# Kernel tuning notes

Hardware: AMD Instinct MI355X
Metric: run time of the kernel (lower is better)

Reference implementation:

```python
import jax, jax.numpy as jnp
import numpy as np

TOP_K = 8
ROUTED_SCALING_FACTOR = 2.5
NORM_TOPK_PROB = True


def setup_inputs() -> dict:
    key = jax.random.key(0)
    k1, k2 = jax.random.split(key)
    hidden_states = jax.random.normal(k1, (4, 4096, 4096), dtype=jnp.float32)
    # gate weight: (n_routed_experts, hidden_size)
    weight = jax.random.normal(k2, (256, 4096), dtype=jnp.float32) * (1.0 / np.sqrt(4096))
    return {"hidden_states": hidden_states, "weight": weight}


def reference(hidden_states, weight):
    bsz, seq_len, h = hidden_states.shape
    x = hidden_states.reshape(-1, h).astype(jnp.float32)  # [T, h]
    # gate logits: [T, E]
    logits = jnp.einsum("th,eh->te", x, weight.astype(jnp.float32))
    scores = jax.nn.softmax(logits, axis=-1)
    topk_weight, topk_idx = jax.lax.top_k(scores, TOP_K)  # [T, k]
    if TOP_K > 1 and NORM_TOPK_PROB:
        denom = jnp.sum(topk_weight, axis=-1, keepdims=True) + 1e-20
        topk_weight = topk_weight / denom * ROUTED_SCALING_FACTOR
    else:
        topk_weight = topk_weight * ROUTED_SCALING_FACTOR
    return (topk_idx, topk_weight)
```

## Files before the change

kernel.cpp:

```cpp
#include <hip/hip_runtime.h>
#include <math.h>

typedef _Float16 half8  __attribute__((ext_vector_type(8)));
typedef _Float16 half4v __attribute__((ext_vector_type(4)));
typedef float    f32x16 __attribute__((ext_vector_type(16)));

namespace {
constexpr int H      = 4096;
constexpr int E      = 256;
constexpr int TOPK   = 8;
constexpr int NCAND  = 12;
constexpr int BM     = 64;
constexpr int BK     = 32;
constexpr int NCHUNK = H / BK;
constexpr int SLD    = E + 4;
constexpr float DELTA = 5e-4f;
constexpr size_t WF_BYTES = (size_t)E * H * 2 * 2;
constexpr int SMEM_BYTES = BM * SLD * 4;
}

__global__ void convert_w_kernel(const float* __restrict__ W,
                                 _Float16* __restrict__ Wf) {
    int t  = blockIdx.x * blockDim.x + threadIdx.x;
    int e  = t >> 10;
    int kq = t & 1023;
    float4 w4 = *(const float4*)(W + ((size_t)e << 12) + (kq << 2));
    float x0 = w4.x * 64.0f, x1 = w4.y * 64.0f, x2 = w4.z * 64.0f, x3 = w4.w * 64.0f;
    _Float16 h0 = (_Float16)x0, h1 = (_Float16)x1, h2 = (_Float16)x2, h3 = (_Float16)x3;
    _Float16 l0 = (_Float16)(x0 - (float)h0), l1 = (_Float16)(x1 - (float)h1);
    _Float16 l2 = (_Float16)(x2 - (float)h2), l3 = (_Float16)(x3 - (float)h3);
    int k    = kq << 2;
    int nt   = e >> 5;
    int ks   = k >> 4;
    int lane = (e & 31) | (((k >> 3) & 1) << 5);
    int j    = k & 7;
    size_t base = (((size_t)nt * 256 + ks) * 2) * 512 + lane * 8 + j;
    half4v hv = {h0, h1, h2, h3};
    half4v lv = {l0, l1, l2, l3};
    *(half4v*)(Wf + base)       = hv;
    *(half4v*)(Wf + base + 512) = lv;
}

struct BF { half8 h[2][2]; half8 l[2][2]; };

__global__ __launch_bounds__(512, 2)
void moe_gate_mfma(const float* __restrict__ X, const _Float16* __restrict__ Wf,
                   const float* __restrict__ Wg,
                   float* __restrict__ out_idx, float* __restrict__ out_w) {
    __shared__ __align__(16) char smem[SMEM_BYTES];
    _Float16* Abuf = (_Float16*)smem;
    float*    sc   = (float*)smem;

    const int tid  = threadIdx.x;
    const int lane = tid & 63;
    const int wave = tid >> 6;
    const int wr   = wave >> 2;
    const int wc   = wave & 3;
    const int m0   = blockIdx.x * BM;

    const int m_s  = tid >> 3;
    const int kq_s = tid & 7;
    const int ks_s = kq_s >> 2;
    const int mt_s = m_s >> 5;
    const int ln_s = (m_s & 31) | (((kq_s >> 1) & 1) << 5);
    const int j_s  = (kq_s & 1) * 4;
    const int dst_s = ((ks_s * 2 + mt_s) * 2) * 512 + ln_s * 8 + j_s;
    const float* xgp = X + (size_t)(m0 + m_s) * H + kq_s * 4;

    f32x16 acc[2];
    #pragma unroll
    for (int nt = 0; nt < 2; ++nt)
        #pragma unroll
        for (int r = 0; r < 16; ++r) acc[nt][r] = 0.0f;

    auto load_b = [&](int kc, BF& b) {
        #pragma unroll
        for (int ks = 0; ks < 2; ++ks)
            #pragma unroll
            for (int nt = 0; nt < 2; ++nt) {
                size_t base = (((size_t)(2 * wc + nt) * 256 + (kc * 2 + ks)) * 2) * 512
                              + lane * 8;
                b.h[ks][nt] = *(const half8*)(Wf + base);
                b.l[ks][nt] = *(const half8*)(Wf + base + 512);
            }
    };
    auto stage = [&](int bufIdx, float4 xv) {
        _Float16* buf = Abuf + bufIdx * 4096;
        float x0 = xv.x, x1 = xv.y, x2 = xv.z, x3 = xv.w;
        _Float16 h0 = (_Float16)x0, h1 = (_Float16)x1, h2 = (_Float16)x2, h3 = (_Float16)x3;
        _Float16 l0 = (_Float16)(x0 - (float)h0), l1 = (_Float16)(x1 - (float)h1);
        _Float16 l2 = (_Float16)(x2 - (float)h2), l3 = (_Float16)(x3 - (float)h3);
        half4v hv = {h0, h1, h2, h3};
        half4v lv = {l0, l1, l2, l3};
        *(half4v*)(buf + dst_s)       = hv;
        *(half4v*)(buf + dst_s + 512) = lv;
    };
    auto compute = [&](int bufIdx, const BF& b) {
        const _Float16* buf = Abuf + bufIdx * 4096;
        #pragma unroll
        for (int ks = 0; ks < 2; ++ks) {
            const _Float16* p = buf + (ks * 2 + wr) * 1024 + lane * 8;
            half8 a_hi = *(const half8*)p;
            half8 a_lo = *(const half8*)(p + 512);
            #pragma unroll
            for (int nt = 0; nt < 2; ++nt) {
                acc[nt] = __builtin_amdgcn_mfma_f32_32x32x16_f16(a_hi, b.h[ks][nt], acc[nt], 0, 0, 0);
                acc[nt] = __builtin_amdgcn_mfma_f32_32x32x16_f16(a_lo, b.h[ks][nt], acc[nt], 0, 0, 0);
                acc[nt] = __builtin_amdgcn_mfma_f32_32x32x16_f16(a_hi, b.l[ks][nt], acc[nt], 0, 0, 0);
            }
        }
    };

    BF bcur;
    load_b(0, bcur);
    float4 xv = *(const float4*)(xgp);
    stage(0, xv);
    __syncthreads();
    float4 xnxt = *(const float4*)(xgp + BK);

    for (int kc = 0; kc < NCHUNK; ++kc) {
        BF bnxt;
        float4 xfar = make_float4(0.f, 0.f, 0.f, 0.f);
        if (kc + 1 < NCHUNK) load_b(kc + 1, bnxt);
        if (kc + 2 < NCHUNK) xfar = *(const float4*)(xgp + (size_t)(kc + 2) * BK);
        compute(kc & 1, bcur);
        if (kc + 1 < NCHUNK) {
            stage((kc + 1) & 1, xnxt);
            asm volatile("s_waitcnt lgkmcnt(0)" ::: "memory");
            __builtin_amdgcn_s_barrier();
        }
        bcur = bnxt;
        xnxt = xfar;
    }

    __syncthreads();
    #pragma unroll
    for (int nt = 0; nt < 2; ++nt) {
        #pragma unroll
        for (int r = 0; r < 16; ++r) {
            int row = (r & 3) + 8 * (r >> 2) + 4 * (lane >> 5);
            int col = lane & 31;
            sc[(wr * 32 + row) * SLD + wc * 64 + nt * 32 + col] = acc[nt][r] * 0.015625f;
        }
    }
    __syncthreads();

    for (int t8 = 0; t8 < 8; ++t8) {
        const int t = wave * 8 + t8;
        float4 pv = *(const float4*)(sc + t * SLD + lane * 4);
        float p0 = pv.x, p1 = pv.y, p2 = pv.z, p3 = pv.w;

        float tv[NCAND]; int ti[NCAND];
        #pragma unroll
        for (int s = 0; s < NCAND; ++s) {
            float bv = p0; int bi = lane * 4;
            if (p1 > bv || (p1 == bv && lane * 4 + 1 < bi)) { bv = p1; bi = lane * 4 + 1; }
            if (p2 > bv || (p2 == bv && lane * 4 + 2 < bi)) { bv = p2; bi = lane * 4 + 2; }
            if (p3 > bv || (p3 == bv && lane * 4 + 3 < bi)) { bv = p3; bi = lane * 4 + 3; }
            #pragma unroll
            for (int off = 32; off > 0; off >>= 1) {
                float ov = __shfl_xor(bv, off, 64);
                int   oi = __shfl_xor(bi, off, 64);
                if (ov > bv || (ov == bv && oi < bi)) { bv = ov; bi = oi; }
            }
            tv[s] = bv; ti[s] = bi;
            if ((bi >> 2) == lane) {
                const int sl = bi & 3;
                if      (sl == 0) p0 = -3e38f;
                else if (sl == 1) p1 = -3e38f;
                else if (sl == 2) p2 = -3e38f;
                else              p3 = -3e38f;
            }
        }

        bool rescue = false;
        #pragma unroll
        for (int g = 0; g < 9; ++g) rescue |= (tv[g] - tv[g + 1] < DELTA);

        if (rescue) {
            double dv[NCAND];
            const float* xr = X + (size_t)(m0 + t) * H;
            #pragma unroll 1
            for (int c = 0; c < NCAND; ++c) {
                const float* wrow = Wg + (size_t)ti[c] * H;
                double s_ = 0.0;
                #pragma unroll
                for (int it = 0; it < 16; ++it) {
                    float4 xa = *(const float4*)(xr + it * 256 + lane * 4);
                    float4 wa = *(const float4*)(wrow + it * 256 + lane * 4);
                    s_ += (double)xa.x * wa.x + (double)xa.y * wa.y
                        + (double)xa.z * wa.z + (double)xa.w * wa.w;
                }
                #pragma unroll
                for (int off = 32; off > 0; off >>= 1) s_ += __shfl_xor(s_, off, 64);
                dv[c] = s_;
            }
            int si[NCAND];
            #pragma unroll
            for (int c = 0; c < NCAND; ++c) si[c] = ti[c];
            #pragma unroll
            for (int a = 0; a < TOPK; ++a) {
                int best = a;
                #pragma unroll
                for (int b = a + 1; b < NCAND; ++b) {
                    if (dv[b] > dv[best] || (dv[b] == dv[best] && si[b] < si[best])) best = b;
                }
                double tdv = dv[a]; dv[a] = dv[best]; dv[best] = tdv;
                int    tsi = si[a]; si[a] = si[best]; si[best] = tsi;
            }
            #pragma unroll
            for (int s = 0; s < TOPK; ++s) { tv[s] = (float)dv[s]; ti[s] = si[s]; }
        }

        if (lane == 0) {
            float M = tv[0];
            float e8[TOPK]; float den = 0.0f;
            #pragma unroll
            for (int s = 0; s < TOPK; ++s) { e8[s] = expf(tv[s] - M); den += e8[s]; }
            float scl = 2.5f / den;
            size_t tok = (size_t)(m0 + t);
            #pragma unroll
            for (int s = 0; s < TOPK; ++s) {
                out_idx[tok * TOPK + s] = (float)ti[s];
                out_w[tok * TOPK + s]   = e8[s] * scl;
            }
        }
    }
}

namespace fb {
constexpr int BM = 32, BK = 32;
constexpr int XS_LD = BM + 4, WS_LD = E + 4;
constexpr int LDS_FLOATS = BK * XS_LD + BK * WS_LD;
}

__global__ __launch_bounds__(256, 2)
void moe_gate_fallback(const float* __restrict__ X, const float* __restrict__ W,
                       float* __restrict__ out_idx, float* __restrict__ out_w) {
    __shared__ float lds[fb::LDS_FLOATS];
    float* xs = lds;
    float* ws = lds + fb::BK * fb::XS_LD;
    const int tid = threadIdx.x;
    const int tx = tid & 31, ty = tid >> 5;
    const int m0 = blockIdx.x * fb::BM;
    float acc[4][8];
    #pragma unroll
    for (int i = 0; i < 4; ++i)
        #pragma unroll
        for (int j = 0; j < 8; ++j) acc[i][j] = 0.0f;
    const int lr = tid >> 3, lc = (tid & 7) * 4;
    const float* xg = X + (size_t)(m0 + lr) * H + lc;
    const float* wg = W + (size_t)lr * H + lc;
    for (int kc = 0; kc < H; kc += fb::BK) {
        float4 xv = *(const float4*)(xg + kc);
        float4 wv[8];
        #pragma unroll
        for (int i = 0; i < 8; ++i) wv[i] = *(const float4*)(wg + (size_t)i * 32 * H + kc);
        __syncthreads();
        #pragma unroll
        for (int j = 0; j < 4; ++j) xs[(lc + j) * fb::XS_LD + lr] = ((const float*)&xv)[j];
        #pragma unroll
        for (int i = 0; i < 8; ++i)
            #pragma unroll
            for (int j = 0; j < 4; ++j)
                ws[(lc + j) * fb::WS_LD + i * 32 + lr] = ((const float*)&wv[i])[j];
        __syncthreads();
        #pragma unroll
        for (int kk = 0; kk < fb::BK; ++kk) {
            float4 xa = *(const float4*)(xs + kk * fb::XS_LD + ty * 4);
            float4 wb0 = *(const float4*)(ws + kk * fb::WS_LD + tx * 8);
            float4 wb1 = *(const float4*)(ws + kk * fb::WS_LD + tx * 8 + 4);
            const float xr[4] = {xa.x, xa.y, xa.z, xa.w};
            const float wr8[8] = {wb0.x, wb0.y, wb0.z, wb0.w, wb1.x, wb1.y, wb1.z, wb1.w};
            #pragma unroll
            for (int i = 0; i < 4; ++i)
                #pragma unroll
                for (int j = 0; j < 8; ++j) acc[i][j] = fmaf(xr[i], wr8[j], acc[i][j]);
        }
    }
    __syncthreads();
    float* sc = lds;
    #pragma unroll
    for (int i = 0; i < 4; ++i) {
        *(float4*)(sc + (ty * 4 + i) * fb::WS_LD + tx * 8) =
            make_float4(acc[i][0], acc[i][1], acc[i][2], acc[i][3]);
        *(float4*)(sc + (ty * 4 + i) * fb::WS_LD + tx * 8 + 4) =
            make_float4(acc[i][4], acc[i][5], acc[i][6], acc[i][7]);
    }
    __syncthreads();
    const int wave = tid >> 6, lane = tid & 63;
    for (int t8 = 0; t8 < 8; ++t8) {
        const int t = wave * 8 + t8;
        float4 pv = *(const float4*)(sc + t * fb::WS_LD + lane * 4);
        float v0 = pv.x, v1 = pv.y, v2 = pv.z, v3 = pv.w;
        float M = fmaxf(fmaxf(v0, v1), fmaxf(v2, v3));
        #pragma unroll
        for (int off = 32; off > 0; off >>= 1) M = fmaxf(M, __shfl_xor(M, off, 64));
        float p0 = expf(v0 - M), p1 = expf(v1 - M), p2 = expf(v2 - M), p3 = expf(v3 - M);
        float z = p0 + p1 + p2 + p3;
        #pragma unroll
        for (int off = 32; off > 0; off >>= 1) z += __shfl_xor(z, off, 64);
        p0 /= z; p1 /= z; p2 /= z; p3 /= z;
        float tv[TOPK]; int ti[TOPK];
        #pragma unroll
        for (int s = 0; s < TOPK; ++s) {
            float bv = p0; int bi = lane * 4;
            if (p1 > bv || (p1 == bv && lane * 4 + 1 < bi)) { bv = p1; bi = lane * 4 + 1; }
            if (p2 > bv || (p2 == bv && lane * 4 + 2 < bi)) { bv = p2; bi = lane * 4 + 2; }
            if (p3 > bv || (p3 == bv && lane * 4 + 3 < bi)) { bv = p3; bi = lane * 4 + 3; }
            #pragma unroll
            for (int off = 32; off > 0; off >>= 1) {
                float ov = __shfl_xor(bv, off, 64);
                int   oi = __shfl_xor(bi, off, 64);
                if (ov > bv || (ov == bv && oi < bi)) { bv = ov; bi = oi; }
            }
            tv[s] = bv; ti[s] = bi;
            if ((bi >> 2) == lane) {
                const int sl = bi & 3;
                if      (sl == 0) p0 = -1.0f;
                else if (sl == 1) p1 = -1.0f;
                else if (sl == 2) p2 = -1.0f;
                else              p3 = -1.0f;
            }
        }
        if (lane == 0) {
            float den = tv[0] + tv[1] + tv[2] + tv[3] + tv[4] + tv[5] + tv[6] + tv[7] + 1e-20f;
            float scl = 2.5f / den;
            size_t tok = (size_t)(m0 + t);
            #pragma unroll
            for (int s = 0; s < TOPK; ++s) {
                out_idx[tok * TOPK + s] = (float)ti[s];
                out_w[tok * TOPK + s]   = tv[s] * scl;
            }
        }
    }
}

extern "C" void kernel_launch(void* const* d_in, const int* in_sizes, int n_in,
                              void* d_out, int out_size, void* d_ws, size_t ws_size,
                              hipStream_t stream) {
    const float* X = (const float*)d_in[0];
    const float* W = (const float*)d_in[1];
    float* out = (float*)d_out;
    const int T = in_sizes[0] / H;
    float* out_idx = out;
    float* out_w   = out + (size_t)T * TOPK;

    if (ws_size >= WF_BYTES && (T % BM) == 0) {
        _Float16* Wf = (_Float16*)d_ws;
        hipLaunchKernelGGL(convert_w_kernel, dim3((E * (H / 4)) / 256), dim3(256), 0, stream, W, Wf);
        hipLaunchKernelGGL(moe_gate_mfma, dim3(T / BM), dim3(512), 0, stream, X, Wf, W, out_idx, out_w);
    } else {
        hipLaunchKernelGGL(moe_gate_fallback, dim3(T / fb::BM), dim3(256), 0, stream, X, W, out_idx, out_w);
    }
}
```

Before: 685.3 us.

## Retile waves to own full M and one expert group, double-chunk pipeline

The wave layout changes from 2x4 (32 rows x 64 experts per wave) to 1x8 (all 64 rows x 32 experts per wave). Each block now fetches the split fp16 weight fragments once rather than twice, which halves global/L2 weight traffic and the B registers each wave holds. The main loop also handles two K-chunks per iteration with four LDS A buffers, so there is one barrier per two chunks. In exchange each wave reads more A fragments from LDS and keeps more X prefetch registers in flight.

Measured after the change: 645.5 us. 5.8% less time.

```diff
diff --git a/kernel.cpp b/kernel.cpp
--- a/kernel.cpp
+++ b/kernel.cpp
@@ -30,18 +30,18 @@
     _Float16 l0 = (_Float16)(x0 - (float)h0), l1 = (_Float16)(x1 - (float)h1);
     _Float16 l2 = (_Float16)(x2 - (float)h2), l3 = (_Float16)(x3 - (float)h3);
     int k    = kq << 2;
-    int nt   = e >> 5;
+    int grp  = e >> 5;
     int ks   = k >> 4;
     int lane = (e & 31) | (((k >> 3) & 1) << 5);
     int j    = k & 7;
-    size_t base = (((size_t)nt * 256 + ks) * 2) * 512 + lane * 8 + j;
+    size_t base = (((size_t)grp * 256 + ks) * 2) * 512 + lane * 8 + j;
     half4v hv = {h0, h1, h2, h3};
     half4v lv = {l0, l1, l2, l3};
     *(half4v*)(Wf + base)       = hv;
     *(half4v*)(Wf + base + 512) = lv;
 }
 
-struct BF { half8 h[2][2]; half8 l[2][2]; };
+struct BF { half8 h[2]; half8 l[2]; };
 
 __global__ __launch_bounds__(512, 2)
 void moe_gate_mfma(const float* __restrict__ X, const _Float16* __restrict__ Wf,
@@ -54,8 +54,6 @@
     const int tid  = threadIdx.x;
     const int lane = tid & 63;
     const int wave = tid >> 6;
-    const int wr   = wave >> 2;
-    const int wc   = wave & 3;
     const int m0   = blockIdx.x * BM;
 
     const int m_s  = tid >> 3;
@@ -69,21 +67,19 @@
 
     f32x16 acc[2];
     #pragma unroll
-    for (int nt = 0; nt < 2; ++nt)
-        #pragma unroll
-        for (int r = 0; r < 16; ++r) acc[nt][r] = 0.0f;
+    for (int mt = 0; mt < 2; ++mt)
+        #pragma unroll
+        for (int r = 0; r < 16; ++r) acc[mt][r] = 0.0f;
 
     auto load_b = [&](int kc, BF& b) {
         #pragma unroll
-        for (int ks = 0; ks < 2; ++ks)
-            #pragma unroll
-            for (int nt = 0; nt < 2; ++nt) {
-                size_t base = (((size_t)(2 * wc + nt) * 256 + (kc * 2 + ks)) * 2) * 512
-                              + lane * 8;
-                b.h[ks][nt] = *(const half8*)(Wf + base);
-                b.l[ks][nt] = *(const half8*)(Wf + base + 512);
-            }
+        for (int ks = 0; ks < 2; ++ks) {
+            size_t base = (((size_t)wave * 256 + (kc * 2 + ks)) * 2) * 512 + lane * 8;
+            b.h[ks] = *(const half8*)(Wf + base);
+            b.l[ks] = *(const half8*)(Wf + base + 512);
+        }
     };
+    auto ldx = [&](int kc) { return *(const float4*)(xgp + (size_t)kc * BK); };
     auto stage = [&](int bufIdx, float4 xv) {
         _Float16* buf = Abuf + bufIdx * 4096;
         float x0 = xv.x, x1 = xv.y, x2 = xv.z, x3 = xv.w;
@@ -98,49 +94,51 @@
     auto compute = [&](int bufIdx, const BF& b) {
         const _Float16* buf = Abuf + bufIdx * 4096;
         #pragma unroll
-        for (int ks = 0; ks < 2; ++ks) {
-            const _Float16* p = buf + (ks * 2 + wr) * 1024 + lane * 8;
-            half8 a_hi = *(const half8*)p;
-            half8 a_lo = *(const half8*)(p + 512);
-            #pragma unroll
-            for (int nt = 0; nt < 2; ++nt) {
-                acc[nt] = __builtin_amdgcn_mfma_f32_32x32x16_f16(a_hi, b.h[ks][nt], acc[nt], 0, 0, 0);
-                acc[nt] = __builtin_amdgcn_mfma_f32_32x32x16_f16(a_lo, b.h[ks][nt], acc[nt], 0, 0, 0);
-                acc[nt] = __builtin_amdgcn_mfma_f32_32x32x16_f16(a_hi, b.l[ks][nt], acc[nt], 0, 0, 0);
-            }
-        }
+        for (int ks = 0; ks < 2; ++ks)
+            #pragma unroll
+            for (int mt = 0; mt < 2; ++mt) {
+                const _Float16* p = buf + (ks * 2 + mt) * 1024 + lane * 8;
+                half8 a_hi = *(const half8*)p;
+                half8 a_lo = *(const half8*)(p + 512);
+                acc[mt] = __builtin_amdgcn_mfma_f32_32x32x16_f16(a_hi, b.h[ks], acc[mt], 0, 0, 0);
+                acc[mt] = __builtin_amdgcn_mfma_f32_32x32x16_f16(a_lo, b.h[ks], acc[mt], 0, 0, 0);
+                acc[mt] = __builtin_amdgcn_mfma_f32_32x32x16_f16(a_hi, b.l[ks], acc[mt], 0, 0, 0);
+            }
     };
 
-    BF bcur;
-    load_b(0, bcur);
-    float4 xv = *(const float4*)(xgp);
-    stage(0, xv);
-    __syncthreads();
-    float4 xnxt = *(const float4*)(xgp + BK);
-
-    for (int kc = 0; kc < NCHUNK; ++kc) {
-        BF bnxt;
-        float4 xfar = make_float4(0.f, 0.f, 0.f, 0.f);
-        if (kc + 1 < NCHUNK) load_b(kc + 1, bnxt);
-        if (kc + 2 < NCHUNK) xfar = *(const float4*)(xgp + (size_t)(kc + 2) * BK);
-        compute(kc & 1, bcur);
-        if (kc + 1 < NCHUNK) {
-            stage((kc + 1) & 1, xnxt);
+    BF b0, b1;
+    load_b(0, b0); load_b(1, b1);
+    stage(0, ldx(0)); stage(1, ldx(1));
+    float4 xc0 = ldx(2), xc1 = ldx(3);
+    __syncthreads();
+
+    #pragma unroll 1
+    for (int i = 0; i < NCHUNK / 2; ++i) {
+        const int kc = 2 * i;
+        BF n0, n1; float4 xn0 = xc0, xn1 = xc1;
+        const bool haveNext = (kc + 2 < NCHUNK);
+        if (haveNext) { load_b(kc + 2, n0); load_b(kc + 3, n1); }
+        if (kc + 4 < NCHUNK) { xn0 = ldx(kc + 4); xn1 = ldx(kc + 5); }
+        compute(kc & 3, b0);
+        compute((kc + 1) & 3, b1);
+        if (haveNext) {
+            stage((kc + 2) & 3, xc0);
+            stage((kc + 3) & 3, xc1);
             asm volatile("s_waitcnt lgkmcnt(0)" ::: "memory");
             __builtin_amdgcn_s_barrier();
-        }
-        bcur = bnxt;
-        xnxt = xfar;
+            b0 = n0; b1 = n1;
+        }
+        xc0 = xn0; xc1 = xn1;
     }
 
     __syncthreads();
     #pragma unroll
-    for (int nt = 0; nt < 2; ++nt) {
+    for (int mt = 0; mt < 2; ++mt) {
         #pragma unroll
         for (int r = 0; r < 16; ++r) {
             int row = (r & 3) + 8 * (r >> 2) + 4 * (lane >> 5);
             int col = lane & 31;
-            sc[(wr * 32 + row) * SLD + wc * 64 + nt * 32 + col] = acc[nt][r] * 0.015625f;
+            sc[(mt * 32 + row) * SLD + wave * 32 + col] = acc[mt][r] * 0.015625f;
         }
     }
     __syncthreads();
```

## Split fused gate kernel into GEMM-to-workspace and separate top-k kernel

Applied to the files above, without the earlier changes.

Splits the fused MFMA GEMM + top-k kernel into two kernels: a GEMM that writes fp32 logits to a workspace buffer, and a separate top-k/rescue kernel that reads them back. The aim is to shrink LDS and register pressure in the GEMM (it no longer needs a score staging buffer) and so raise occupancy and overlap. The cost is an extra global write and read of T*E logits plus one more kernel launch. The new path runs only when the workspace is large enough.

New measurement: 702.3 us. +2.5%, slower.

```diff
diff --git a/kernel.cpp b/kernel.cpp
--- a/kernel.cpp
+++ b/kernel.cpp
@@ -30,11 +30,11 @@
     _Float16 l0 = (_Float16)(x0 - (float)h0), l1 = (_Float16)(x1 - (float)h1);
     _Float16 l2 = (_Float16)(x2 - (float)h2), l3 = (_Float16)(x3 - (float)h3);
     int k    = kq << 2;
-    int nt   = e >> 5;
+    int grp  = e >> 5;
     int ks   = k >> 4;
     int lane = (e & 31) | (((k >> 3) & 1) << 5);
     int j    = k & 7;
-    size_t base = (((size_t)nt * 256 + ks) * 2) * 512 + lane * 8 + j;
+    size_t base = (((size_t)grp * 256 + ks) * 2) * 512 + lane * 8 + j;
     half4v hv = {h0, h1, h2, h3};
     half4v lv = {l0, l1, l2, l3};
     *(half4v*)(Wf + base)       = hv;
@@ -42,6 +42,208 @@
 }
 
 struct BF { half8 h[2][2]; half8 l[2][2]; };
+
+__global__ __launch_bounds__(512, 2)
+void moe_gate_gemm(const float* __restrict__ X, const _Float16* __restrict__ Wf,
+                   float* __restrict__ Lg) {
+    __shared__ __align__(16) _Float16 Abuf[2 * 4096];
+
+    const int tid  = threadIdx.x;
+    const int lane = tid & 63;
+    const int wave = tid >> 6;
+    const int wr   = wave >> 2;
+    const int wc   = wave & 3;
+    const int m0   = blockIdx.x * BM;
+
+    const int m_s  = tid >> 3;
+    const int kq_s = tid & 7;
+    const int ks_s = kq_s >> 2;
+    const int mt_s = m_s >> 5;
+    const int ln_s = (m_s & 31) | (((kq_s >> 1) & 1) << 5);
+    const int j_s  = (kq_s & 1) * 4;
+    const int dst_s = ((ks_s * 2 + mt_s) * 2) * 512 + ln_s * 8 + j_s;
+    const float* xgp = X + (size_t)(m0 + m_s) * H + kq_s * 4;
+
+    f32x16 acc[2];
+    #pragma unroll
+    for (int nt = 0; nt < 2; ++nt)
+        #pragma unroll
+        for (int r = 0; r < 16; ++r) acc[nt][r] = 0.0f;
+
+    auto load_b = [&](int kc, BF& b) {
+        #pragma unroll
+        for (int ks = 0; ks < 2; ++ks)
+            #pragma unroll
+            for (int nt = 0; nt < 2; ++nt) {
+                size_t base = (((size_t)(2 * wc + nt) * 256 + (kc * 2 + ks)) * 2) * 512
+                              + lane * 8;
+                b.h[ks][nt] = *(const half8*)(Wf + base);
+                b.l[ks][nt] = *(const half8*)(Wf + base + 512);
+            }
+    };
+    auto ldx = [&](int kc) { return *(const float4*)(xgp + (size_t)kc * BK); };
+    auto stage = [&](int bufIdx, float4 xv) {
+        _Float16* buf = Abuf + bufIdx * 4096;
+        float x0 = xv.x, x1 = xv.y, x2 = xv.z, x3 = xv.w;
+        _Float16 h0 = (_Float16)x0, h1 = (_Float16)x1, h2 = (_Float16)x2, h3 = (_Float16)x3;
+        _Float16 l0 = (_Float16)(x0 - (float)h0), l1 = (_Float16)(x1 - (float)h1);
+        _Float16 l2 = (_Float16)(x2 - (float)h2), l3 = (_Float16)(x3 - (float)h3);
+        half4v hv = {h0, h1, h2, h3};
+        half4v lv = {l0, l1, l2, l3};
+        *(half4v*)(buf + dst_s)       = hv;
+        *(half4v*)(buf + dst_s + 512) = lv;
+    };
+    auto compute = [&](int bufIdx, const BF& b) {
+        const _Float16* buf = Abuf + bufIdx * 4096;
+        #pragma unroll
+        for (int ks = 0; ks < 2; ++ks) {
+            const _Float16* p = buf + (ks * 2 + wr) * 1024 + lane * 8;
+            half8 a_hi = *(const half8*)p;
+            half8 a_lo = *(const half8*)(p + 512);
+            #pragma unroll
+            for (int nt = 0; nt < 2; ++nt) {
+                acc[nt] = __builtin_amdgcn_mfma_f32_32x32x16_f16(a_hi, b.h[ks][nt], acc[nt], 0, 0, 0);
+                acc[nt] = __builtin_amdgcn_mfma_f32_32x32x16_f16(a_lo, b.h[ks][nt], acc[nt], 0, 0, 0);
+                acc[nt] = __builtin_amdgcn_mfma_f32_32x32x16_f16(a_hi, b.l[ks][nt], acc[nt], 0, 0, 0);
+            }
+        }
+    };
+
+    BF b0;
+    load_b(0, b0);
+    stage(0, ldx(0));
+    __syncthreads();
+    float4 x1 = ldx(1);
+
+    #pragma unroll 1
+    for (int i = 0; i < NCHUNK / 2; ++i) {
+        const int kc = 2 * i;
+        BF b1;
+        load_b(kc + 1, b1);
+        float4 x2 = make_float4(0.f, 0.f, 0.f, 0.f);
+        if (kc + 2 < NCHUNK) x2 = ldx(kc + 2);
+        compute(kc & 1, b0);
+        stage((kc + 1) & 1, x1);
+        asm volatile("s_waitcnt lgkmcnt(0)" ::: "memory");
+        __builtin_amdgcn_s_barrier();
+        if (kc + 2 < NCHUNK) {
+            load_b(kc + 2, b0);
+            float4 x3 = make_float4(0.f, 0.f, 0.f, 0.f);
+            if (kc + 3 < NCHUNK) x3 = ldx(kc + 3);
+            compute((kc + 1) & 1, b1);
+            stage((kc + 2) & 1, x2);
+            asm volatile("s_waitcnt lgkmcnt(0)" ::: "memory");
+            __builtin_amdgcn_s_barrier();
+            x1 = x3;
+        } else {
+            compute((kc + 1) & 1, b1);
+        }
+    }
+
+    float* Lrow = Lg + (size_t)m0 * E;
+    #pragma unroll
+    for (int nt = 0; nt < 2; ++nt) {
+        #pragma unroll
+        for (int r = 0; r < 16; ++r) {
+            int row = (r & 3) + 8 * (r >> 2) + 4 * (lane >> 5);
+            int col = lane & 31;
+            Lrow[(size_t)(wr * 32 + row) * E + wc * 64 + nt * 32 + col] =
+                acc[nt][r] * 0.015625f;
+        }
+    }
+}
+
+__global__ __launch_bounds__(512, 2)
+void moe_gate_topk(const float* __restrict__ X, const float* __restrict__ Wg,
+                   const float* __restrict__ Lg,
+                   float* __restrict__ out_idx, float* __restrict__ out_w) {
+    const int tid  = threadIdx.x;
+    const int lane = tid & 63;
+    const int wave = tid >> 6;
+    const int m0   = blockIdx.x * BM;
+
+    for (int t8 = 0; t8 < 8; ++t8) {
+        const int t   = wave * 8 + t8;
+        const int tok = m0 + t;
+        float4 pv = *(const float4*)(Lg + (size_t)tok * E + lane * 4);
+        float p0 = pv.x, p1 = pv.y, p2 = pv.z, p3 = pv.w;
+
+        float tv[NCAND]; int ti[NCAND];
+        #pragma unroll
+        for (int s = 0; s < NCAND; ++s) {
+            float bv = p0; int bi = lane * 4;
+            if (p1 > bv || (p1 == bv && lane * 4 + 1 < bi)) { bv = p1; bi = lane * 4 + 1; }
+            if (p2 > bv || (p2 == bv && lane * 4 + 2 < bi)) { bv = p2; bi = lane * 4 + 2; }
+            if (p3 > bv || (p3 == bv && lane * 4 + 3 < bi)) { bv = p3; bi = lane * 4 + 3; }
+            #pragma unroll
+            for (int off = 32; off > 0; off >>= 1) {
+                float ov = __shfl_xor(bv, off, 64);
+                int   oi = __shfl_xor(bi, off, 64);
+                if (ov > bv || (ov == bv && oi < bi)) { bv = ov; bi = oi; }
+            }
+            tv[s] = bv; ti[s] = bi;
+            if ((bi >> 2) == lane) {
+                const int sl = bi & 3;
+                if      (sl == 0) p0 = -3e38f;
+                else if (sl == 1) p1 = -3e38f;
+                else if (sl == 2) p2 = -3e38f;
+                else              p3 = -3e38f;
+            }
+        }
+
+        bool rescue = false;
+        #pragma unroll
+        for (int g = 0; g < 9; ++g) rescue |= (tv[g] - tv[g + 1] < DELTA);
+
+        if (rescue) {
+            double dv[NCAND];
+            const float* xr = X + (size_t)tok * H;
+            #pragma unroll 1
+            for (int c = 0; c < NCAND; ++c) {
+                const float* wrow = Wg + (size_t)ti[c] * H;
+                double s_ = 0.0;
+                #pragma unroll
+                for (int it = 0; it < 16; ++it) {
+                    float4 xa = *(const float4*)(xr + it * 256 + lane * 4);
+                    float4 wa = *(const float4*)(wrow + it * 256 + lane * 4);
+                    s_ += (double)xa.x * wa.x + (double)xa.y * wa.y
+                        + (double)xa.z * wa.z + (double)xa.w * wa.w;
+                }
+                #pragma unroll
+                for (int off = 32; off > 0; off >>= 1) s_ += __shfl_xor(s_, off, 64);
+                dv[c] = s_;
+            }
+            int si[NCAND];
+            #pragma unroll
+            for (int c = 0; c < NCAND; ++c) si[c] = ti[c];
+            #pragma unroll
+            for (int a = 0; a < TOPK; ++a) {
+                int best = a;
+                #pragma unroll
+                for (int b = a + 1; b < NCAND; ++b) {
+                    if (dv[b] > dv[best] || (dv[b] == dv[best] && si[b] < si[best])) best = b;
+                }
+                double tdv = dv[a]; dv[a] = dv[best]; dv[best] = tdv;
+                int    tsi = si[a]; si[a] = si[best]; si[best] = tsi;
+            }
+            #pragma unroll
+            for (int s = 0; s < TOPK; ++s) { tv[s] = (float)dv[s]; ti[s] = si[s]; }
+        }
+
+        if (lane == 0) {
+            float M = tv[0];
+            float e8[TOPK]; float den = 0.0f;
+            #pragma unroll
+            for (int s = 0; s < TOPK; ++s) { e8[s] = expf(tv[s] - M); den += e8[s]; }
+            float scl = 2.5f / den;
+            #pragma unroll
+            for (int s = 0; s < TOPK; ++s) {
+                out_idx[(size_t)tok * TOPK + s] = (float)ti[s];
+                out_w[(size_t)tok * TOPK + s]   = e8[s] * scl;
+            }
+        }
+    }
+}
 
 __global__ __launch_bounds__(512, 2)
 void moe_gate_mfma(const float* __restrict__ X, const _Float16* __restrict__ Wf,
@@ -345,8 +547,15 @@
     const int T = in_sizes[0] / H;
     float* out_idx = out;
     float* out_w   = out + (size_t)T * TOPK;
-
-    if (ws_size >= WF_BYTES && (T % BM) == 0) {
+    const size_t LG_BYTES = (size_t)T * E * sizeof(float);
+
+    if (ws_size >= WF_BYTES + LG_BYTES && (T % BM) == 0) {
+        _Float16* Wf = (_Float16*)d_ws;
+        float*    Lg = (float*)((char*)d_ws + WF_BYTES);
+        hipLaunchKernelGGL(convert_w_kernel, dim3((E * (H / 4)) / 256), dim3(256), 0, stream, W, Wf);
+        hipLaunchKernelGGL(moe_gate_gemm, dim3(T / BM), dim3(512), 0, stream, X, Wf, Lg);
+        hipLaunchKernelGGL(moe_gate_topk, dim3(T / BM), dim3(512), 0, stream, X, W, Lg, out_idx, out_w);
+    } else if (ws_size >= WF_BYTES && (T % BM) == 0) {
         _Float16* Wf = (_Float16*)d_ws;
         hipLaunchKernelGGL(convert_w_kernel, dim3((E * (H / 4)) / 256), dim3(256), 0, stream, W, Wf);
         hipLaunchKernelGGL(moe_gate_mfma, dim3(T / BM), dim3(512), 0, stream, X, Wf, W, out_idx, out_w);
```

## Split top-k selection into 16-lane groups handling four tokens per wave

Applied to the files above, without the earlier changes.

Restructures the per-token top-12 candidate selection so that each wave processes four tokens at once, with each 16-lane group owning one token and each lane holding 16 scores. This cuts the butterfly reduction from six shuffle steps to four and halves the serial token iterations. The candidates are staged in extra shared memory and then read back for the existing rescue and output logic. The cost is more registers per lane, a 16-way rescan after each pick, and a larger LDS footprint that could affect occupancy.

Result: faster. 651.7 us (-4.9%).

```diff
diff --git a/kernel.cpp b/kernel.cpp
--- a/kernel.cpp
+++ b/kernel.cpp
@@ -16,7 +16,8 @@
 constexpr int SLD    = E + 4;
 constexpr float DELTA = 5e-4f;
 constexpr size_t WF_BYTES = (size_t)E * H * 2 * 2;
-constexpr int SMEM_BYTES = BM * SLD * 4;
+constexpr int SC_BYTES   = BM * SLD * 4;
+constexpr int SMEM_BYTES = SC_BYTES + BM * NCAND * 8;
 }
 
 __global__ void convert_w_kernel(const float* __restrict__ W,
@@ -50,6 +51,8 @@
     __shared__ __align__(16) char smem[SMEM_BYTES];
     _Float16* Abuf = (_Float16*)smem;
     float*    sc   = (float*)smem;
+    float*    tvS  = (float*)(smem + SC_BYTES);
+    int*      tiS  = (int*)  (smem + SC_BYTES + BM * NCAND * 4);
 
     const int tid  = threadIdx.x;
     const int lane = tid & 63;
@@ -145,32 +148,62 @@
     }
     __syncthreads();
 
+    const int l16 = lane & 15;
+    const int grp = lane >> 4;
+    #pragma unroll 1
+    for (int b = 0; b < 2; ++b) {
+        const int t = wave * 8 + b * 4 + grp;
+        float v[16];
+        #pragma unroll
+        for (int q = 0; q < 4; ++q) {
+            float4 f = *(const float4*)(sc + t * SLD + l16 * 16 + q * 4);
+            v[q * 4 + 0] = f.x; v[q * 4 + 1] = f.y;
+            v[q * 4 + 2] = f.z; v[q * 4 + 3] = f.w;
+        }
+        float bv = v[0]; int bi = l16 * 16;
+        #pragma unroll
+        for (int j = 1; j < 16; ++j)
+            if (v[j] > bv) { bv = v[j]; bi = l16 * 16 + j; }
+
+        float tv[NCAND]; int ti[NCAND];
+        #pragma unroll
+        for (int s = 0; s < NCAND; ++s) {
+            float wv = bv; int wi = bi;
+            #pragma unroll
+            for (int off = 8; off > 0; off >>= 1) {
+                float ov = __shfl_xor(wv, off, 64);
+                int   oi = __shfl_xor(wi, off, 64);
+                if (ov > wv || (ov == wv && oi < wi)) { wv = ov; wi = oi; }
+            }
+            tv[s] = wv; ti[s] = wi;
+            if ((wi >> 4) == l16) {
+                const int slot = wi & 15;
+                #pragma unroll
+                for (int j = 0; j < 16; ++j)
+                    if (slot == j) v[j] = -3e38f;
+                bv = v[0]; bi = l16 * 16;
+                #pragma unroll
+                for (int j = 1; j < 16; ++j)
+                    if (v[j] > bv) { bv = v[j]; bi = l16 * 16 + j; }
+            }
+        }
+        if (l16 == 0) {
+            #pragma unroll
+            for (int s = 0; s < NCAND; ++s) {
+                tvS[t * NCAND + s] = tv[s];
+                tiS[t * NCAND + s] = ti[s];
+            }
+        }
+    }
+    asm volatile("s_waitcnt lgkmcnt(0)" ::: "memory");
+
     for (int t8 = 0; t8 < 8; ++t8) {
         const int t = wave * 8 + t8;
-        float4 pv = *(const float4*)(sc + t * SLD + lane * 4);
-        float p0 = pv.x, p1 = pv.y, p2 = pv.z, p3 = pv.w;
-
         float tv[NCAND]; int ti[NCAND];
         #pragma unroll
         for (int s = 0; s < NCAND; ++s) {
-            float bv = p0; int bi = lane * 4;
-            if (p1 > bv || (p1 == bv && lane * 4 + 1 < bi)) { bv = p1; bi = lane * 4 + 1; }
-            if (p2 > bv || (p2 == bv && lane * 4 + 2 < bi)) { bv = p2; bi = lane * 4 + 2; }
-            if (p3 > bv || (p3 == bv && lane * 4 + 3 < bi)) { bv = p3; bi = lane * 4 + 3; }
-            #pragma unroll
-            for (int off = 32; off > 0; off >>= 1) {
-                float ov = __shfl_xor(bv, off, 64);
-                int   oi = __shfl_xor(bi, off, 64);
-                if (ov > bv || (ov == bv && oi < bi)) { bv = ov; bi = oi; }
-            }
-            tv[s] = bv; ti[s] = bi;
-            if ((bi >> 2) == lane) {
-                const int sl = bi & 3;
-                if      (sl == 0) p0 = -3e38f;
-                else if (sl == 1) p1 = -3e38f;
-                else if (sl == 2) p2 = -3e38f;
-                else              p3 = -3e38f;
-            }
+            tv[s] = tvS[t * NCAND + s];
+            ti[s] = tiS[t * NCAND + s];
         }
 
         bool rescue = false;
```
